# Kernel tuning notes

Measured on AMD Instinct MI355X. Metric: run time of the kernel, lower is better.

The kernel has to match this reference:

```python
import jax, jax.numpy as jnp
import numpy as np

EPS = 1e-5

def _conv1x1(x, w, b):
    # x: [B,C,...], w: [O,C], b: [O]
    y = jnp.einsum('oc,bc...->bo...', w, x)
    return y + b.reshape((1, -1) + (1,) * (x.ndim - 2))

def _bn(x, g, be, m, v):
    # inference-mode BatchNorm with running stats (PyTorch eps=1e-5)
    s = (1, -1) + (1,) * (x.ndim - 2)
    return (x - m.reshape(s)) * (g.reshape(s) / jnp.sqrt(v.reshape(s) + EPS)) + be.reshape(s)

def _patches3x3(x):
    # F.unfold(kernel=3, pad=1, stride=1, dil=1): [B,C,H,W] -> [B,C,9,H,W], row-major kernel order
    B, C, H, W = x.shape
    xp = jnp.pad(x, ((0, 0), (0, 0), (1, 1), (1, 1)))
    return jnp.stack([xp[:, :, ky:ky + H, kx:kx + W] for ky in range(3) for kx in range(3)], axis=2)

def setup_inputs() -> dict:
    key = jax.random.key(0)
    ks = jax.random.split(key, 40)
    B, Cin, H, W = 4, 16, 192, 192
    Cm = 64  # mlp[-1]
    d = {}
    d['x'] = jax.random.normal(ks[0], (B, Cin, H, W), jnp.float32)
    d['group_mask'] = jnp.ones((B, 1, H, W), jnp.float32)
    d['group_xyz'] = jax.random.normal(ks[1], (B, 3, 9, H, W), jnp.float32)
    def bnp(k, c):
        k1, k2, k3, k4 = jax.random.split(k, 4)
        return (1.0 + 0.1 * jax.random.normal(k1, (c,)), 0.1 * jax.random.normal(k2, (c,)),
                0.1 * jax.random.normal(k3, (c,)), 0.5 + jax.random.uniform(k4, (c,)))
    d['w0'] = 0.1 * jax.random.normal(ks[2], (Cm, Cin)); d['b0'] = 0.01 * jax.random.normal(ks[3], (Cm,))
    d['g0'], d['beta0'], d['m0'], d['v0'] = bnp(ks[4], Cm)
    wn_dims = [(8, 3), (8, 8), (16, 8)]
    for i, (o, c) in enumerate(wn_dims):
        d[f'wn_w{i}'] = 0.3 * jax.random.normal(ks[5 + 3 * i], (o, c))
        d[f'wn_b{i}'] = 0.01 * jax.random.normal(ks[6 + 3 * i], (o,))
        d[f'wn_g{i}'], d[f'wn_beta{i}'], d[f'wn_m{i}'], d[f'wn_v{i}'] = bnp(ks[7 + 3 * i], o)
    d['lw'] = 0.05 * jax.random.normal(ks[20], (Cm, 16 * Cm)); d['lb'] = 0.01 * jax.random.normal(ks[21], (Cm,))
    d['lg'], d['lbeta'], d['lm'], d['lv'] = bnp(ks[22], Cm)
    return d

def reference(x, group_mask, group_xyz,
              w0, b0, g0, beta0, m0, v0,
              wn_w0, wn_b0, wn_g0, wn_beta0, wn_m0, wn_v0,
              wn_w1, wn_b1, wn_g1, wn_beta1, wn_m1, wn_v1,
              wn_w2, wn_b2, wn_g2, wn_beta2, wn_m2, wn_v2,
              lw, lb, lg, lbeta, lm, lv):
    # mlp_convs chain (single layer here)
    x = jax.nn.relu(_bn(_conv1x1(x, w0, b0), g0, beta0, m0, v0))  # [B,Cm,H,W]
    B, _, N, H, W = group_xyz.shape
    # WeightNet on local coords: [B,3,N,H*W] -> [B,16,N,H*W]
    gz = group_xyz.reshape(B, 3, N, H * W)
    for w, b, g, be, m, v in ((wn_w0, wn_b0, wn_g0, wn_beta0, wn_m0, wn_v0),
                              (wn_w1, wn_b1, wn_g1, wn_beta1, wn_m1, wn_v1),
                              (wn_w2, wn_b2, wn_g2, wn_beta2, wn_m2, wn_v2)):
        gz = jax.nn.relu(_bn(_conv1x1(gz, w, b), g, be, m, v))
    gz = gz.reshape(B, 16, N, H, W)
    p = _patches3x3(x)  # [B,Cm,9,H,W]
    C = p.shape[1]
    # per-pixel matmul: [B,H,W,C,9] @ [B,H,W,9,16] -> [B,H,W,C,16]
    out = jnp.einsum('bckhw,bokhw->bhwco', p, gz)
    out = out.reshape(B, H, W, C * 16).transpose(0, 3, 1, 2)  # [B,16*Cm,H,W]
    return jax.nn.relu(_bn(_conv1x1(out, lw, lb), lg, lbeta, lm, lv))
```

## Files before the change

### kernel.cpp

```cpp
#include <hip/hip_runtime.h>
#include <hip/hip_bf16.h>

#define HH 192
#define WW 192
#define HWPROD (192*192)
#define EPSBN 1e-5f

typedef _Float16 f16x8 __attribute__((ext_vector_type(8)));
typedef _Float16 f16x4 __attribute__((ext_vector_type(4)));
typedef _Float16 f16x2 __attribute__((ext_vector_type(2)));
typedef float f32x4 __attribute__((ext_vector_type(4)));

__global__ void prep_k(const float* __restrict__ w0, const float* __restrict__ b0,
                       const float* __restrict__ g0, const float* __restrict__ beta0,
                       const float* __restrict__ m0, const float* __restrict__ v0,
                       const float* __restrict__ wnw0, const float* __restrict__ wnb0,
                       const float* __restrict__ wng0, const float* __restrict__ wnbe0,
                       const float* __restrict__ wnm0, const float* __restrict__ wnv0,
                       const float* __restrict__ wnw1, const float* __restrict__ wnb1,
                       const float* __restrict__ wng1, const float* __restrict__ wnbe1,
                       const float* __restrict__ wnm1, const float* __restrict__ wnv1,
                       const float* __restrict__ wnw2, const float* __restrict__ wnb2,
                       const float* __restrict__ wng2, const float* __restrict__ wnbe2,
                       const float* __restrict__ wnm2, const float* __restrict__ wnv2,
                       const float* __restrict__ lw, const float* __restrict__ lb,
                       const float* __restrict__ lg, const float* __restrict__ lbeta,
                       const float* __restrict__ lm, const float* __restrict__ lv,
                       _Float16* __restrict__ whF,
                       float* __restrict__ lbf,
                       float* __restrict__ w0f, float* __restrict__ b0f,
                       float* __restrict__ wnP)
{
    int idx = blockIdx.x * 256 + threadIdx.x;
    if (idx < 65536) {
        int j    = idx & 7;
        int lane = (idx >> 3) & 63;
        int kg   = (idx >> 9) & 31;
        int nt   = idx >> 14;
        int k = kg * 32 + ((lane >> 4) & 3) * 8 + j;
        int n = nt * 16 + (lane & 15);
        float s = lg[n] * rsqrtf(lv[n] + EPSBN);
        whF[idx] = (_Float16)(lw[n * 1024 + k] * s);
    } else if (idx < 65600) {
        int j = idx - 65536;
        float s = lg[j] * rsqrtf(lv[j] + EPSBN);
        lbf[j] = (lb[j] - lm[j]) * s + lbeta[j];
    } else if (idx < 66624) {
        int t = idx - 65600;
        int o = t >> 4;
        float s = g0[o] * rsqrtf(v0[o] + EPSBN);
        w0f[t] = w0[t] * s;
    } else if (idx < 66688) {
        int o = idx - 66624;
        float s = g0[o] * rsqrtf(v0[o] + EPSBN);
        b0f[o] = (b0[o] - m0[o]) * s + beta0[o];
    } else if (idx < 66936) {
        int t = idx - 66688;
        if (t < 24)       { int o = t / 3;           float s = wng0[o] * rsqrtf(wnv0[o] + EPSBN); wnP[t] = wnw0[t] * s; }
        else if (t < 32)  { int o = t - 24;          float s = wng0[o] * rsqrtf(wnv0[o] + EPSBN); wnP[t] = (wnb0[o] - wnm0[o]) * s + wnbe0[o]; }
        else if (t < 96)  { int t2 = t - 32;  int o = t2 >> 3; float s = wng1[o] * rsqrtf(wnv1[o] + EPSBN); wnP[t] = wnw1[t2] * s; }
        else if (t < 104) { int o = t - 96;          float s = wng1[o] * rsqrtf(wnv1[o] + EPSBN); wnP[t] = (wnb1[o] - wnm1[o]) * s + wnbe1[o]; }
        else if (t < 232) { int t2 = t - 104; int o = t2 >> 3; float s = wng2[o] * rsqrtf(wnv2[o] + EPSBN); wnP[t] = wnw2[t2] * s; }
        else              { int o = t - 232;         float s = wng2[o] * rsqrtf(wnv2[o] + EPSBN); wnP[t] = (wnb2[o] - wnm2[o]) * s + wnbe2[o]; }
    }
}

__global__ __launch_bounds__(256) void conv0_k(const float* __restrict__ x,
                                               const float* __restrict__ w0f,
                                               const float* __restrict__ b0f,
                                               _Float16* __restrict__ x1L)
{
    const int pix = blockIdx.x * 256 + threadIdx.x;
    const int b = pix / HWPROD;
    const int p = pix - b * HWPROD;

    float xv[16];
#pragma unroll
    for (int cin = 0; cin < 16; cin++)
        xv[cin] = x[((size_t)b * 16 + cin) * HWPROD + p];

    _Float16* outp = x1L + (size_t)pix * 64;
#pragma unroll
    for (int co = 0; co < 64; co += 4) {
        f32x4 a = { b0f[co], b0f[co + 1], b0f[co + 2], b0f[co + 3] };
#pragma unroll
        for (int cin = 0; cin < 16; cin++) {
            float xc = xv[cin];
            a.x += w0f[(co + 0) * 16 + cin] * xc;
            a.y += w0f[(co + 1) * 16 + cin] * xc;
            a.z += w0f[(co + 2) * 16 + cin] * xc;
            a.w += w0f[(co + 3) * 16 + cin] * xc;
        }
        a.x = fmaxf(a.x, 0.f); a.y = fmaxf(a.y, 0.f);
        a.z = fmaxf(a.z, 0.f); a.w = fmaxf(a.w, 0.f);
        *(f16x4*)(outp + co) = __builtin_convertvector(a, f16x4);
    }
}

__global__ __launch_bounds__(512, 4) void pconv_main_k(const float* __restrict__ gxyz,
                                                       const _Float16* __restrict__ x1L,
                                                       const _Float16* __restrict__ whF,
                                                       const float* __restrict__ lbf,
                                                       const float* __restrict__ wnP,
                                                       float* __restrict__ out)
{
    __shared__ __align__(16) char smem[58496];
    f16x2*    xtP = reinterpret_cast<f16x2*>(smem);
    _Float16* A0  = reinterpret_cast<_Float16*>(smem + 25728);
    _Float16* A1  = reinterpret_cast<_Float16*>(smem + 42112);
    _Float16* gzF = reinterpret_cast<_Float16*>(smem + 25728);
    float*    Cb  = reinterpret_cast<float*>(smem);

    const int tid = threadIdx.x;
    const int bid = blockIdx.x;
    const int b   = bid / (HH * 3);
    const int rem = bid % (HH * 3);
    const int h   = rem / 3;
    const int wc0 = (rem % 3) * 64;

    for (int q = tid; q < 1584; q += 512) {
        int c8   = q & 7;
        int colr = q >> 3;
        int col  = colr % 66;
        int r    = colr / 66;
        int hr = h + r - 1;
        int wc = wc0 + col - 1;
        union { f16x8 v; f16x2 p[4]; } U;
        U.v = f16x8{};
        if (hr >= 0 && hr < HH && wc >= 0 && wc < WW) {
            U.v = *(const f16x8*)(x1L + (((size_t)b * HH + hr) * WW + wc) * 64 + c8 * 8);
        }
#pragma unroll
        for (int i = 0; i < 4; i++)
            xtP[(c8 * 4 + i) * 201 + colr] = U.p[i];
    }

    for (int u = tid; u < 576; u += 512) {
        int pixu = u & 63, tap = u >> 6;
        size_t base = ((size_t)(b * 3) * 9 + tap) * HWPROD + (size_t)h * WW + wc0 + pixu;
        float z0 = gxyz[base];
        float z1 = gxyz[base + (size_t)9 * HWPROD];
        float z2 = gxyz[base + (size_t)18 * HWPROD];
        float h0[8], h1[8];
#pragma unroll
        for (int o = 0; o < 8; o++) {
            float a = wnP[24 + o] + wnP[o * 3 + 0] * z0 + wnP[o * 3 + 1] * z1 + wnP[o * 3 + 2] * z2;
            h0[o] = fmaxf(a, 0.f);
        }
#pragma unroll
        for (int o = 0; o < 8; o++) {
            float a = wnP[96 + o];
#pragma unroll
            for (int c = 0; c < 8; c++) a += wnP[32 + o * 8 + c] * h0[c];
            h1[o] = fmaxf(a, 0.f);
        }
        float g[16];
#pragma unroll
        for (int o = 0; o < 16; o++) {
            float a = wnP[232 + o];
#pragma unroll
            for (int c = 0; c < 8; c++) a += wnP[104 + o * 8 + c] * h1[c];
            g[o] = fmaxf(a, 0.f);
        }
        f16x8 lo, hi;
#pragma unroll
        for (int o = 0; o < 8; o++) { lo[o] = (_Float16)g[o]; hi[o] = (_Float16)g[o + 8]; }
        *(f16x8*)&gzF[pixu * 152 + tap * 16]     = lo;
        *(f16x8*)&gzF[pixu * 152 + tap * 16 + 8] = hi;
    }
    __syncthreads();

    const int pix = tid & 63;
    const int u8  = tid >> 6;
    const int oh  = u8 & 1;
    const int cp  = u8 >> 1;
    const int lane = tid & 63;
    const int wv   = tid >> 6;
    const int nt   = wv & 3;
    const int mt2  = wv >> 2;

    f16x2 gq2[9][4];
#pragma unroll
    for (int t = 0; t < 9; t++) {
        union { f16x8 v; f16x2 h[4]; } G;
        G.v = *(const f16x8*)&gzF[pix * 152 + t * 16 + oh * 8];
#pragma unroll
        for (int d = 0; d < 4; d++) gq2[t][d] = G.h[d];
    }
    __syncthreads();

    const int mt = pix >> 4;

    auto phase1 = [&](int cc, _Float16* Ab) {
        union { f16x2 h2[4]; f16x8 v; } av0, av1;
#pragma unroll
        for (int d = 0; d < 4; d++) { av0.h2[d] = f16x2{0, 0}; av1.h2[d] = f16x2{0, 0}; }
        const f16x2* xrow = xtP + (cc * 4 + cp) * 201 + pix;
#pragma unroll
        for (int ky = 0; ky < 3; ky++) {
#pragma unroll
            for (int kx = 0; kx < 3; kx++) {
                const int t = ky * 3 + kx;
                f16x2 xq = xrow[ky * 66 + kx];
                f16x2 xb0 = __builtin_shufflevector(xq, xq, 0, 0);
                f16x2 xb1 = __builtin_shufflevector(xq, xq, 1, 1);
#pragma unroll
                for (int d = 0; d < 4; d++) {
                    av0.h2[d] = __builtin_elementwise_fma(xb0, gq2[t][d], av0.h2[d]);
                    av1.h2[d] = __builtin_elementwise_fma(xb1, gq2[t][d], av1.h2[d]);
                }
            }
        }
        const int row = cp * 4 + mt;
        *(f16x8*)&Ab[(row * 64 + (pix & 15) + 16 * oh) * 8]       = av0.v;
        *(f16x8*)&Ab[(row * 64 + (pix & 15) + 16 * (2 + oh)) * 8] = av1.v;
    };

    const f16x8* whF8 = (const f16x8*)whF;
    f32x4 facc[2];
    facc[0] = f32x4{0.f, 0.f, 0.f, 0.f};
    facc[1] = f32x4{0.f, 0.f, 0.f, 0.f};

    phase1(0, A0);
    __syncthreads();

#pragma unroll 2
    for (int cc = 0; cc < 8; cc++) {
        const _Float16* Ac = (cc & 1) ? A1 : A0;
#pragma unroll
        for (int kb = 0; kb < 4; kb++) {
            const int kg = cc * 4 + kb;
            f16x8 a0 = *(const f16x8*)&Ac[((kb * 4 + 2 * mt2) * 64 + lane) * 8];
            f16x8 a1 = *(const f16x8*)&Ac[((kb * 4 + 2 * mt2 + 1) * 64 + lane) * 8];
            f16x8 wh = whF8[((nt * 32 + kg) << 6) + lane];
            facc[0] = __builtin_amdgcn_mfma_f32_16x16x32_f16(a0, wh, facc[0], 0, 0, 0);
            facc[1] = __builtin_amdgcn_mfma_f32_16x16x32_f16(a1, wh, facc[1], 0, 0, 0);
        }
        if (cc < 7) phase1(cc + 1, (cc & 1) ? A0 : A1);
        __syncthreads();
    }

    {
        const int n = nt * 16 + (lane & 15);
        const float bias = lbf[n];
#pragma unroll
        for (int m = 0; m < 2; m++) {
            const int pixm = (2 * mt2 + m) * 16 + (lane >> 4) * 4;
#pragma unroll
            for (int r = 0; r < 4; r++)
                Cb[n * 67 + pixm + r] = fmaxf(facc[m][r] + bias, 0.f);
        }
    }
    __syncthreads();
    {
        const int pixq = tid & 63, jq = tid >> 6;
        size_t ob = ((size_t)b * 64 + jq * 8) * HWPROD + (size_t)h * WW + wc0 + pixq;
#pragma unroll
        for (int i = 0; i < 8; i++) {
            out[ob + (size_t)i * HWPROD] = Cb[(jq * 8 + i) * 67 + pixq];
        }
    }
}

extern "C" void kernel_launch(void* const* d_in, const int* in_sizes, int n_in,
                              void* d_out, int out_size, void* d_ws, size_t ws_size,
                              hipStream_t stream) {
    const float* x    = (const float*)d_in[0];
    const float* gxyz = (const float*)d_in[2];

    char* ws = (char*)d_ws;
    _Float16* x1L = (_Float16*)ws;
    _Float16* whF = x1L + 9437184;
    float* lbf = (float*)(whF + 65536);
    float* w0f = lbf + 64;
    float* b0f = w0f + 1024;
    float* wnP = b0f + 64;

    prep_k<<<262, 256, 0, stream>>>(
        (const float*)d_in[3],  (const float*)d_in[4],  (const float*)d_in[5],
        (const float*)d_in[6],  (const float*)d_in[7],  (const float*)d_in[8],
        (const float*)d_in[9],  (const float*)d_in[10], (const float*)d_in[11],
        (const float*)d_in[12], (const float*)d_in[13], (const float*)d_in[14],
        (const float*)d_in[15], (const float*)d_in[16], (const float*)d_in[17],
        (const float*)d_in[18], (const float*)d_in[19], (const float*)d_in[20],
        (const float*)d_in[21], (const float*)d_in[22], (const float*)d_in[23],
        (const float*)d_in[24], (const float*)d_in[25], (const float*)d_in[26],
        (const float*)d_in[27], (const float*)d_in[28], (const float*)d_in[29],
        (const float*)d_in[30], (const float*)d_in[31], (const float*)d_in[32],
        whF, lbf, w0f, b0f, wnP);

    conv0_k<<<576, 256, 0, stream>>>(x, w0f, b0f, x1L);

    pconv_main_k<<<4 * HH * 3, 512, 0, stream>>>(gxyz, x1L, whF, lbf, wnP,
                                                 (float*)d_out);
}
```

Measured before the change: 220.9 us.

## Fuse first 1x1 conv into main kernel, computing halo activations on the fly

Removes the separate conv0 kernel and its fp16 intermediate buffer in global memory. Each block now loads the raw fp32 input for a 3x66 halo tile into shared memory and computes the 64-channel conv+BN+ReLU per halo pixel itself. This avoids writing and re-reading about 19 MB of intermediate data and one kernel launch. In exchange, halo pixels are recomputed by neighbouring blocks (about 3x redundant compute), shared memory use grows, and the weight-net stage is reordered before the tile build.

Result: slower. 226.7 us (+2.6%).

```diff
diff --git a/kernel.cpp b/kernel.cpp
--- a/kernel.cpp
+++ b/kernel.cpp
@@ -65,50 +65,23 @@
     }
 }
 
-__global__ __launch_bounds__(256) void conv0_k(const float* __restrict__ x,
-                                               const float* __restrict__ w0f,
-                                               const float* __restrict__ b0f,
-                                               _Float16* __restrict__ x1L)
-{
-    const int pix = blockIdx.x * 256 + threadIdx.x;
-    const int b = pix / HWPROD;
-    const int p = pix - b * HWPROD;
-
-    float xv[16];
-#pragma unroll
-    for (int cin = 0; cin < 16; cin++)
-        xv[cin] = x[((size_t)b * 16 + cin) * HWPROD + p];
-
-    _Float16* outp = x1L + (size_t)pix * 64;
-#pragma unroll
-    for (int co = 0; co < 64; co += 4) {
-        f32x4 a = { b0f[co], b0f[co + 1], b0f[co + 2], b0f[co + 3] };
-#pragma unroll
-        for (int cin = 0; cin < 16; cin++) {
-            float xc = xv[cin];
-            a.x += w0f[(co + 0) * 16 + cin] * xc;
-            a.y += w0f[(co + 1) * 16 + cin] * xc;
-            a.z += w0f[(co + 2) * 16 + cin] * xc;
-            a.w += w0f[(co + 3) * 16 + cin] * xc;
-        }
-        a.x = fmaxf(a.x, 0.f); a.y = fmaxf(a.y, 0.f);
-        a.z = fmaxf(a.z, 0.f); a.w = fmaxf(a.w, 0.f);
-        *(f16x4*)(outp + co) = __builtin_convertvector(a, f16x4);
-    }
-}
-
 __global__ __launch_bounds__(512, 4) void pconv_main_k(const float* __restrict__ gxyz,
-                                                       const _Float16* __restrict__ x1L,
+                                                       const float* __restrict__ x,
                                                        const _Float16* __restrict__ whF,
                                                        const float* __restrict__ lbf,
                                                        const float* __restrict__ wnP,
+                                                       const float* __restrict__ w0f,
+                                                       const float* __restrict__ b0f,
                                                        float* __restrict__ out)
 {
-    __shared__ __align__(16) char smem[58496];
+    __shared__ __align__(16) char smem[62848];
     f16x2*    xtP = reinterpret_cast<f16x2*>(smem);
     _Float16* A0  = reinterpret_cast<_Float16*>(smem + 25728);
     _Float16* A1  = reinterpret_cast<_Float16*>(smem + 42112);
     _Float16* gzF = reinterpret_cast<_Float16*>(smem + 25728);
+    float*    xS  = reinterpret_cast<float*>(smem + 45184);
+    float*    wSt = reinterpret_cast<float*>(smem + 58496);
+    float*    bS  = reinterpret_cast<float*>(smem + 62592);
     float*    Cb  = reinterpret_cast<float*>(smem);
 
     const int tid = threadIdx.x;
@@ -117,6 +90,58 @@
     const int rem = bid % (HH * 3);
     const int h   = rem / 3;
     const int wc0 = (rem % 3) * 64;
+
+    for (int t = tid; t < 1024; t += 512)
+        wSt[(t & 15) * 64 + (t >> 4)] = w0f[t];
+    if (tid < 64) bS[tid] = b0f[tid];
+
+    for (int i = tid; i < 3168; i += 512) {
+        int ci   = i / 198;
+        int colr = i - ci * 198;
+        int col  = colr % 66;
+        int r    = colr / 66;
+        int hr = h + r - 1;
+        int wc = wc0 + col - 1;
+        float v = 0.f;
+        if (hr >= 0 && hr < HH && wc >= 0 && wc < WW)
+            v = x[((size_t)(b * 16 + ci) * HH + hr) * WW + wc];
+        xS[ci * 198 + colr] = v;
+    }
+
+    for (int u = tid; u < 576; u += 512) {
+        int pixu = u & 63, tap = u >> 6;
+        size_t base = ((size_t)(b * 3) * 9 + tap) * HWPROD + (size_t)h * WW + wc0 + pixu;
+        float z0 = gxyz[base];
+        float z1 = gxyz[base + (size_t)9 * HWPROD];
+        float z2 = gxyz[base + (size_t)18 * HWPROD];
+        float h0[8], h1[8];
+#pragma unroll
+        for (int o = 0; o < 8; o++) {
+            float a = wnP[24 + o] + wnP[o * 3 + 0] * z0 + wnP[o * 3 + 1] * z1 + wnP[o * 3 + 2] * z2;
+            h0[o] = fmaxf(a, 0.f);
+        }
+#pragma unroll
+        for (int o = 0; o < 8; o++) {
+            float a = wnP[96 + o];
+#pragma unroll
+            for (int c = 0; c < 8; c++) a += wnP[32 + o * 8 + c] * h0[c];
+            h1[o] = fmaxf(a, 0.f);
+        }
+        float g[16];
+#pragma unroll
+        for (int o = 0; o < 16; o++) {
+            float a = wnP[232 + o];
+#pragma unroll
+            for (int c = 0; c < 8; c++) a += wnP[104 + o * 8 + c] * h1[c];
+            g[o] = fmaxf(a, 0.f);
+        }
+        f16x8 lo, hi;
+#pragma unroll
+        for (int o = 0; o < 8; o++) { lo[o] = (_Float16)g[o]; hi[o] = (_Float16)g[o + 8]; }
+        *(f16x8*)&gzF[pixu * 152 + tap * 16]     = lo;
+        *(f16x8*)&gzF[pixu * 152 + tap * 16 + 8] = hi;
+    }
+    __syncthreads();
 
     for (int q = tid; q < 1584; q += 512) {
         int c8   = q & 7;
@@ -125,48 +150,28 @@
         int r    = colr / 66;
         int hr = h + r - 1;
         int wc = wc0 + col - 1;
-        union { f16x8 v; f16x2 p[4]; } U;
-        U.v = f16x8{};
+        f16x2 p0 = f16x2{0, 0}, p1 = f16x2{0, 0}, p2 = f16x2{0, 0}, p3 = f16x2{0, 0};
         if (hr >= 0 && hr < HH && wc >= 0 && wc < WW) {
-            U.v = *(const f16x8*)(x1L + (((size_t)b * HH + hr) * WW + wc) * 64 + c8 * 8);
-        }
-#pragma unroll
-        for (int i = 0; i < 4; i++)
-            xtP[(c8 * 4 + i) * 201 + colr] = U.p[i];
-    }
-
-    for (int u = tid; u < 576; u += 512) {
-        int pixu = u & 63, tap = u >> 6;
-        size_t base = ((size_t)(b * 3) * 9 + tap) * HWPROD + (size_t)h * WW + wc0 + pixu;
-        float z0 = gxyz[base];
-        float z1 = gxyz[base + (size_t)9 * HWPROD];
-        float z2 = gxyz[base + (size_t)18 * HWPROD];
-        float h0[8], h1[8];
-#pragma unroll
-        for (int o = 0; o < 8; o++) {
-            float a = wnP[24 + o] + wnP[o * 3 + 0] * z0 + wnP[o * 3 + 1] * z1 + wnP[o * 3 + 2] * z2;
-            h0[o] = fmaxf(a, 0.f);
-        }
-#pragma unroll
-        for (int o = 0; o < 8; o++) {
-            float a = wnP[96 + o];
-#pragma unroll
-            for (int c = 0; c < 8; c++) a += wnP[32 + o * 8 + c] * h0[c];
-            h1[o] = fmaxf(a, 0.f);
-        }
-        float g[16];
-#pragma unroll
-        for (int o = 0; o < 16; o++) {
-            float a = wnP[232 + o];
-#pragma unroll
-            for (int c = 0; c < 8; c++) a += wnP[104 + o * 8 + c] * h1[c];
-            g[o] = fmaxf(a, 0.f);
-        }
-        f16x8 lo, hi;
-#pragma unroll
-        for (int o = 0; o < 8; o++) { lo[o] = (_Float16)g[o]; hi[o] = (_Float16)g[o + 8]; }
-        *(f16x8*)&gzF[pixu * 152 + tap * 16]     = lo;
-        *(f16x8*)&gzF[pixu * 152 + tap * 16 + 8] = hi;
+            f32x4 acc0 = *(const f32x4*)&bS[c8 * 8];
+            f32x4 acc1 = *(const f32x4*)&bS[c8 * 8 + 4];
+#pragma unroll
+            for (int ci = 0; ci < 16; ci++) {
+                float xv = xS[ci * 198 + colr];
+                f32x4 xb = {xv, xv, xv, xv};
+                f32x4 w0v = *(const f32x4*)&wSt[ci * 64 + c8 * 8];
+                f32x4 w1v = *(const f32x4*)&wSt[ci * 64 + c8 * 8 + 4];
+                acc0 = __builtin_elementwise_fma(xb, w0v, acc0);
+                acc1 = __builtin_elementwise_fma(xb, w1v, acc1);
+            }
+            p0 = f16x2{(_Float16)fmaxf(acc0[0], 0.f), (_Float16)fmaxf(acc0[1], 0.f)};
+            p1 = f16x2{(_Float16)fmaxf(acc0[2], 0.f), (_Float16)fmaxf(acc0[3], 0.f)};
+            p2 = f16x2{(_Float16)fmaxf(acc1[0], 0.f), (_Float16)fmaxf(acc1[1], 0.f)};
+            p3 = f16x2{(_Float16)fmaxf(acc1[2], 0.f), (_Float16)fmaxf(acc1[3], 0.f)};
+        }
+        xtP[(c8 * 4 + 0) * 201 + colr] = p0;
+        xtP[(c8 * 4 + 1) * 201 + colr] = p1;
+        xtP[(c8 * 4 + 2) * 201 + colr] = p2;
+        xtP[(c8 * 4 + 3) * 201 + colr] = p3;
     }
     __syncthreads();
 
@@ -269,8 +274,7 @@
     const float* gxyz = (const float*)d_in[2];
 
     char* ws = (char*)d_ws;
-    _Float16* x1L = (_Float16*)ws;
-    _Float16* whF = x1L + 9437184;
+    _Float16* whF = (_Float16*)ws;
     float* lbf = (float*)(whF + 65536);
     float* w0f = lbf + 64;
     float* b0f = w0f + 1024;
@@ -289,8 +293,6 @@
         (const float*)d_in[30], (const float*)d_in[31], (const float*)d_in[32],
         whF, lbf, w0f, b0f, wnP);
 
-    conv0_k<<<576, 256, 0, stream>>>(x, w0f, b0f, x1L);
-
-    pconv_main_k<<<4 * HH * 3, 512, 0, stream>>>(gxyz, x1L, whF, lbf, wnP,
-                                                 (float*)d_out);
+    pconv_main_k<<<4 * HH * 3, 512, 0, stream>>>(gxyz, x, whF, lbf, wnP,
+                                                 w0f, b0f, (float*)d_out);
 }
```
